# Kernel tuning notes

Hardware: AMD Instinct MI355X
Metric: run time of the kernel (lower is better)

Reference implementation:

```python
import jax, jax.numpy as jnp
import numpy as np

THRESHOLD = 0.9  # graph_threshold; graph_secondary is None
EPS = 1e-12


def setup_inputs() -> dict:
    key = jax.random.key(0)
    k_x, k_cw, k_cb, k_u, k_lw, k_lb = jax.random.split(key, 6)
    B = 8192
    x = jax.random.normal(k_x, (B, 1, 28, 28), dtype=jnp.float32)
    conv_w = jax.random.normal(k_cw, (4, 1, 2, 2), dtype=jnp.float32) * 0.5  # OIHW
    conv_b = jax.random.normal(k_cb, (4,), dtype=jnp.float32) * 0.1
    # random orthogonal 4x4 "quantum" unitary via QR, as in the torch buffer
    unitary = jnp.linalg.qr(jax.random.normal(k_u, (4, 4), dtype=jnp.float32))[0]
    D = 4 * 14 * 14  # conv_out * num_patches = 784
    lin_w = jax.random.normal(k_lw, (10, D), dtype=jnp.float32) * (1.0 / np.sqrt(D))
    lin_b = jax.random.normal(k_lb, (10,), dtype=jnp.float32) * 0.01
    return {"x": x, "conv_w": conv_w, "conv_b": conv_b, "unitary": unitary,
            "lin_w": lin_w, "lin_b": lin_b}


def _forward(x, conv_w, conv_b, unitary, lin_w, lin_b):
    B = x.shape[0]
    # _PatchConv: 2x2 conv, stride 2, then flatten to [B, 4*14*14]
    feats = jax.lax.conv_general_dilated(
        x, conv_w, window_strides=(2, 2), padding="VALID",
        dimension_numbers=("NCHW", "OIHW", "NCHW"))
    feats = feats + conv_b[None, :, None, None]
    flat = feats.reshape(B, -1)                      # [B, 784]
    # _QuantumPatchEncoder: reinterpret as [B, 196, 4], apply unitary^T
    patches = flat.reshape(B, -1, 4)
    qf = jnp.einsum("bnk,wk->bnw", patches, unitary).reshape(B, -1)  # [B, 784]
    # linear head + log_softmax
    logits = qf @ lin_w.T + lin_b
    log_probs = jax.nn.log_softmax(logits, axis=-1)
    # GraphAdjacencyLayer: pairwise squared-cosine fidelity, thresholded.
    # Vectorized: normalize rows, one GEMM, square, threshold.
    qn = qf / (jnp.linalg.norm(qf, axis=-1, keepdims=True) + EPS)   # [B, 784]
    fid = (qn @ qn.T) ** 2                                          # [B, B]
    adj = jnp.where(fid >= THRESHOLD, 1.0, 0.0).astype(jnp.float32)
    adj = adj * (1.0 - jnp.eye(B, dtype=jnp.float32))  # no self-edges (i<j pairs)
    return log_probs, adj


def reference(x, conv_w, conv_b, unitary, lin_w, lin_b):
    return _forward(x, conv_w, conv_b, unitary, lin_w, lin_b)
```

## Files before the change

kernel.cpp:

```cpp
#include <hip/hip_runtime.h>
#include <hip/hip_bf16.h>

typedef unsigned char uchar_t;
typedef __attribute__((ext_vector_type(4))) float f32x4;

#define B_SZ 8192
#define D_FT 784
#define K_PAD 832
#define N_KT 13
#define THRESH 0.9f

#define GLOBAL_AS(p) ((const __attribute__((address_space(1))) void*)(p))
#define LDS_AS(p)    ((__attribute__((address_space(3))) void*)(p))

__global__ __launch_bounds__(256) void preproc_kernel(
    const float* __restrict__ x, const float* __restrict__ conv_w,
    const float* __restrict__ conv_b, const float* __restrict__ unitary,
    const float* __restrict__ lin_w, const float* __restrict__ lin_b,
    float* __restrict__ log_probs, uchar_t* __restrict__ qn)
{
    __shared__ float xr[4][784];
    __shared__ float qf[4][784];

    const int t = threadIdx.x, lane = t & 63, wave = t >> 6;
    const int b = blockIdx.x * 4 + wave;
    float* xw = xr[wave];
    float* qw = qf[wave];

    const float4* xsrc = (const float4*)(x + (size_t)b * 784);
    #pragma unroll
    for (int i = lane; i < 196; i += 64) ((float4*)xw)[i] = xsrc[i];
    __syncthreads();

    float sumsq = 0.f;
    for (int g = lane; g < 196; g += 64) {
        const int c = g / 49, p = g % 49;
        const float w00 = conv_w[c*4+0], w01 = conv_w[c*4+1];
        const float w10 = conv_w[c*4+2], w11 = conv_w[c*4+3];
        const float bcv = conv_b[c];
        float feat[4];
        #pragma unroll
        for (int j = 0; j < 4; ++j) {
            const int s = 4*p + j;
            const int h = s / 14, wq = s % 14;
            const float* px = &xw[(2*h)*28 + 2*wq];
            feat[j] = bcv + w00*px[0] + w01*px[1] + w10*px[28] + w11*px[29];
        }
        #pragma unroll
        for (int w = 0; w < 4; ++w) {
            float v = unitary[w*4+0]*feat[0] + unitary[w*4+1]*feat[1]
                    + unitary[w*4+2]*feat[2] + unitary[w*4+3]*feat[3];
            qw[4*g + w] = v;
            sumsq += v * v;
        }
    }
    __syncthreads();

    #pragma unroll
    for (int off = 1; off < 64; off <<= 1) sumsq += __shfl_xor(sumsq, off, 64);
    const float inv = 1.0f / (sqrtf(sumsq) + 1e-12f);

    unsigned int* qrow = (unsigned int*)(qn + (size_t)b * K_PAD);
    for (int i = lane; i < 208; i += 64) {
        unsigned int o = 0u;
        if (i < 196) {
            const float v0 = qw[4*i+0] * inv, v1 = qw[4*i+1] * inv;
            const float v2 = qw[4*i+2] * inv, v3 = qw[4*i+3] * inv;
            int lo = __builtin_amdgcn_cvt_pk_fp8_f32(v0, v1, 0, 0);
            o = (unsigned int)__builtin_amdgcn_cvt_pk_fp8_f32(v2, v3, lo, 1);
        }
        qrow[i] = o;
    }

    float acc[10];
    #pragma unroll
    for (int cl = 0; cl < 10; ++cl) acc[cl] = 0.f;
    for (int k = lane; k < 784; k += 64) {
        const float v = qw[k];
        #pragma unroll
        for (int cl = 0; cl < 10; ++cl) acc[cl] += v * lin_w[cl*784 + k];
    }
    #pragma unroll
    for (int cl = 0; cl < 10; ++cl) {
        #pragma unroll
        for (int off = 1; off < 64; off <<= 1)
            acc[cl] += __shfl_xor(acc[cl], off, 64);
        acc[cl] += lin_b[cl];
    }
    if (lane == 0) {
        float mx = -1e30f;
        #pragma unroll
        for (int cl = 0; cl < 10; ++cl) mx = fmaxf(mx, acc[cl]);
        float se = 0.f;
        #pragma unroll
        for (int cl = 0; cl < 10; ++cl) se += expf(acc[cl] - mx);
        const float lse = mx + logf(se);
        #pragma unroll
        for (int cl = 0; cl < 10; ++cl)
            log_probs[(size_t)b*10 + cl] = acc[cl] - lse;
    }
}

__global__ __launch_bounds__(256, 4) void gram_kernel(
    const uchar_t* __restrict__ qn, float* __restrict__ adj)
{
    const int t0 = blockIdx.x;
    int tl = (t0 & 7) * 260 + (t0 >> 3);
    int br = (int)((129.0 - sqrt(16641.0 - 8.0 * (double)tl)) * 0.5);
    while ((br + 1) * (129 - (br + 1)) / 2 <= tl) ++br;
    while (br * (129 - br) / 2 > tl) --br;
    const int bc = br + (tl - br * (129 - br) / 2);

    __shared__ uchar_t ldsA[3][8192] __attribute__((aligned(16)));
    __shared__ uchar_t ldsB[3][8192] __attribute__((aligned(16)));

    const int t = threadIdx.x;
    const int lane = t & 63, wave = t >> 6;
    const int wr = wave >> 1, wc = wave & 1;
    const int quad = lane >> 4, l16 = lane & 15;

    const int srow = lane & 15, sck = (lane >> 4) * 16;
    const uchar_t* gA0 = qn + (size_t)(br*128 + wave*16     + srow) * K_PAD + sck;
    const uchar_t* gA1 = qn + (size_t)(br*128 + (wave+4)*16 + srow) * K_PAD + sck;
    const uchar_t* gB0 = qn + (size_t)(bc*128 + wave*16     + srow) * K_PAD + sck;
    const uchar_t* gB1 = qn + (size_t)(bc*128 + (wave+4)*16 + srow) * K_PAD + sck;
    const int ld0 = wave * 1024, ld1 = (wave + 4) * 1024;

    #define STAGE(p, koff) do {                                                            \
        __builtin_amdgcn_global_load_lds(GLOBAL_AS(gA0 + (koff)), LDS_AS(&ldsA[p][ld0]), 16, 0, 0); \
        __builtin_amdgcn_global_load_lds(GLOBAL_AS(gA1 + (koff)), LDS_AS(&ldsA[p][ld1]), 16, 0, 0); \
        __builtin_amdgcn_global_load_lds(GLOBAL_AS(gB0 + (koff)), LDS_AS(&ldsB[p][ld0]), 16, 0, 0); \
        __builtin_amdgcn_global_load_lds(GLOBAL_AS(gB1 + (koff)), LDS_AS(&ldsB[p][ld1]), 16, 0, 0); \
    } while (0)

    f32x4 acc[4][4] = {};
    STAGE(0, 0);
    STAGE(1, 64);

    #pragma unroll
    for (int kt = 0; kt < N_KT; ++kt) {
        const int p = kt % 3, p2 = (kt + 2) % 3;

        asm volatile("" ::: "memory");
        if (kt + 1 < N_KT) {
            __builtin_amdgcn_s_waitcnt(0xF74);
        } else {
            __builtin_amdgcn_s_waitcnt(0xF70);
        }
        __builtin_amdgcn_s_barrier();
        asm volatile("" ::: "memory");

        if (kt + 2 < N_KT) STAGE(p2, (kt + 2) * 64);
        asm volatile("" ::: "memory");

        #pragma unroll
        for (int s = 0; s < 2; ++s) {
            const int fo = (2*s + (quad >> 1))*256 + l16*16 + (quad & 1)*8;
            long bfr[4];
            #pragma unroll
            for (int ni = 0; ni < 4; ++ni)
                bfr[ni] = *(const long*)&ldsB[p][(wc*4 + ni)*1024 + fo];
            #pragma unroll
            for (int mi = 0; mi < 4; ++mi) {
                const long af = *(const long*)&ldsA[p][(wr*4 + mi)*1024 + fo];
                #pragma unroll
                for (int ni = 0; ni < 4; ++ni)
                    acc[mi][ni] = __builtin_amdgcn_mfma_f32_16x16x32_fp8_fp8(
                        af, bfr[ni], acc[mi][ni], 0, 0, 0);
            }
        }
    }
    #undef STAGE

    const bool offdiag = (br != bc);
    #pragma unroll
    for (int mi = 0; mi < 4; ++mi) {
        const int gr0 = br*128 + wr*64 + mi*16 + quad*4;
        #pragma unroll
        for (int ni = 0; ni < 4; ++ni) {
            const int gc = bc*128 + wc*64 + ni*16 + l16;
            const f32x4 v = acc[mi][ni];
            float o[4];
            #pragma unroll
            for (int r = 0; r < 4; ++r)
                o[r] = (v[r]*v[r] >= THRESH && (gr0 + r) != gc) ? 1.0f : 0.0f;
            #pragma unroll
            for (int r = 0; r < 4; ++r)
                __builtin_nontemporal_store(o[r], &adj[(size_t)(gr0 + r) * B_SZ + gc]);
            if (offdiag) {
                f32x4 ov = { o[0], o[1], o[2], o[3] };
                __builtin_nontemporal_store(ov, (f32x4*)&adj[(size_t)gc * B_SZ + gr0]);
            }
        }
    }
}

extern "C" void kernel_launch(void* const* d_in, const int* in_sizes, int n_in,
                              void* d_out, int out_size, void* d_ws, size_t ws_size,
                              hipStream_t stream) {
    const float* x       = (const float*)d_in[0];
    const float* conv_w  = (const float*)d_in[1];
    const float* conv_b  = (const float*)d_in[2];
    const float* unitary = (const float*)d_in[3];
    const float* lin_w   = (const float*)d_in[4];
    const float* lin_b   = (const float*)d_in[5];

    float* log_probs = (float*)d_out;
    float* adj       = (float*)d_out + (size_t)B_SZ * 10;
    uchar_t* qn      = (uchar_t*)d_ws;

    preproc_kernel<<<B_SZ / 4, 256, 0, stream>>>(x, conv_w, conv_b, unitary,
                                                 lin_w, lin_b, log_probs, qn);
    gram_kernel<<<2080, 256, 0, stream>>>(qn, adj);
}
```

Before: 359.4 us.

## Pre-zero adjacency and store only wavefront tiles with edges; double-buffer LDS

```diff
diff --git a/kernel.cpp b/kernel.cpp
--- a/kernel.cpp
+++ b/kernel.cpp
@@ -12,6 +12,16 @@
 
 #define GLOBAL_AS(p) ((const __attribute__((address_space(1))) void*)(p))
 #define LDS_AS(p)    ((__attribute__((address_space(3))) void*)(p))
+
+__global__ __launch_bounds__(256) void zero_adj_kernel(float* __restrict__ adj)
+{
+    const size_t n4 = (size_t)B_SZ * B_SZ / 4;
+    f32x4 z = {0.f, 0.f, 0.f, 0.f};
+    f32x4* p = (f32x4*)adj;
+    for (size_t i = (size_t)blockIdx.x * 256 + threadIdx.x; i < n4;
+         i += (size_t)gridDim.x * 256)
+        __builtin_nontemporal_store(z, p + i);
+}
 
 __global__ __launch_bounds__(256) void preproc_kernel(
     const float* __restrict__ x, const float* __restrict__ conv_w,
@@ -111,8 +121,8 @@
     while (br * (129 - br) / 2 > tl) --br;
     const int bc = br + (tl - br * (129 - br) / 2);
 
-    __shared__ uchar_t ldsA[3][8192] __attribute__((aligned(16)));
-    __shared__ uchar_t ldsB[3][8192] __attribute__((aligned(16)));
+    __shared__ uchar_t ldsA[2][8192] __attribute__((aligned(16)));
+    __shared__ uchar_t ldsB[2][8192] __attribute__((aligned(16)));
 
     const int t = threadIdx.x;
     const int lane = t & 63, wave = t >> 6;
@@ -135,22 +145,17 @@
 
     f32x4 acc[4][4] = {};
     STAGE(0, 0);
-    STAGE(1, 64);
 
     #pragma unroll
     for (int kt = 0; kt < N_KT; ++kt) {
-        const int p = kt % 3, p2 = (kt + 2) % 3;
+        const int p = kt & 1;
 
         asm volatile("" ::: "memory");
-        if (kt + 1 < N_KT) {
-            __builtin_amdgcn_s_waitcnt(0xF74);
-        } else {
-            __builtin_amdgcn_s_waitcnt(0xF70);
-        }
+        __builtin_amdgcn_s_waitcnt(0xF70);
         __builtin_amdgcn_s_barrier();
         asm volatile("" ::: "memory");
 
-        if (kt + 2 < N_KT) STAGE(p2, (kt + 2) * 64);
+        if (kt + 1 < N_KT) STAGE(p ^ 1, (kt + 1) * 64);
         asm volatile("" ::: "memory");
 
         #pragma unroll
@@ -181,15 +186,19 @@
             const int gc = bc*128 + wc*64 + ni*16 + l16;
             const f32x4 v = acc[mi][ni];
             float o[4];
+            bool h = false;
             #pragma unroll
-            for (int r = 0; r < 4; ++r)
+            for (int r = 0; r < 4; ++r) {
                 o[r] = (v[r]*v[r] >= THRESH && (gr0 + r) != gc) ? 1.0f : 0.0f;
-            #pragma unroll
-            for (int r = 0; r < 4; ++r)
-                __builtin_nontemporal_store(o[r], &adj[(size_t)(gr0 + r) * B_SZ + gc]);
-            if (offdiag) {
-                f32x4 ov = { o[0], o[1], o[2], o[3] };
-                __builtin_nontemporal_store(ov, (f32x4*)&adj[(size_t)gc * B_SZ + gr0]);
+                h = h || (o[r] != 0.0f);
+            }
+            if (__any(h)) {
+                #pragma unroll
+                for (int r = 0; r < 4; ++r)
+                    adj[(size_t)(gr0 + r) * B_SZ + gc] = o[r];
+                if (offdiag)
+                    *(float4*)&adj[(size_t)gc * B_SZ + gr0] =
+                        make_float4(o[0], o[1], o[2], o[3]);
             }
         }
     }
@@ -209,6 +218,7 @@
     float* adj       = (float*)d_out + (size_t)B_SZ * 10;
     uchar_t* qn      = (uchar_t*)d_ws;
 
+    zero_adj_kernel<<<4096, 256, 0, stream>>>(adj);
     preproc_kernel<<<B_SZ / 4, 256, 0, stream>>>(x, conv_w, conv_b, unitary,
                                                  lin_w, lin_b, log_probs, qn);
     gram_kernel<<<2080, 256, 0, stream>>>(qn, adj);
```

Measured after the change: 373.6 us. 1.04x slower.
